# Optimization experiments

Measured on AMD Instinct MI355X. Metric: run time of the kernel, lower is better.

The kernel has to match this reference:

```python
import jax, jax.numpy as jnp
import numpy as np

I, H, O = 256, 512, 256  # input_size, hidden_size, output_size
B, S = 4096, 50


def _lstm_cell(x_t, h, c, Wih, Whh, bih, bhh):
    # torch gate order: i, f, g, o
    gates = x_t @ Wih.T + h @ Whh.T + bih + bhh  # [B, 4H]
    i, f, g, o = jnp.split(gates, 4, axis=-1)
    i = jax.nn.sigmoid(i)
    f = jax.nn.sigmoid(f)
    g = jnp.tanh(g)
    o = jax.nn.sigmoid(o)
    c_new = f * c + i * g
    h_new = o * jnp.tanh(c_new)
    return h_new, c_new


def setup_inputs() -> dict:
    key = jax.random.key(0)
    ks = jax.random.split(key, 12)
    s_i = 1.0 / np.sqrt(H)  # torch LSTM/Linear init scale
    u = lambda k, shape: jax.random.uniform(k, shape, jnp.float32, -s_i, s_i)
    return {
        "x": jax.random.normal(ks[0], (B, S, I), jnp.float32),
        "enc_Wih": u(ks[1], (4 * H, I)),
        "enc_Whh": u(ks[2], (4 * H, H)),
        "enc_bih": u(ks[3], (4 * H,)),
        "enc_bhh": u(ks[4], (4 * H,)),
        "dec_Wih": u(ks[5], (4 * H, I)),
        "dec_Whh": u(ks[6], (4 * H, H)),
        "dec_bih": u(ks[7], (4 * H,)),
        "dec_bhh": u(ks[8], (4 * H,)),
        "fc_W": u(ks[9], (O, H)),
        "fc_b": u(ks[10], (O,)),
        "target_seq_length": 20,
    }


def reference(x, enc_Wih, enc_Whh, enc_bih, enc_bhh,
              dec_Wih, dec_Whh, dec_bih, dec_bhh,
              fc_W, fc_b, target_seq_length):
    batch = x.shape[0]
    h0 = jnp.zeros((batch, H), x.dtype)
    c0 = jnp.zeros((batch, H), x.dtype)

    # ---- encoder: scan over time ----
    def enc_step(carry, x_t):
        h, c = carry
        h, c = _lstm_cell(x_t, h, c, enc_Wih, enc_Whh, enc_bih, enc_bhh)
        return (h, c), None

    (h, c), _ = jax.lax.scan(enc_step, (h0, c0), jnp.swapaxes(x, 0, 1))

    dec_in0 = jnp.zeros((batch, I), x.dtype)

    def dec_step(carry, _):
        h, c, inp = carry
        h, c = _lstm_cell(inp, h, c, dec_Wih, dec_Whh, dec_bih, dec_bhh)
        out = h @ fc_W.T + fc_b  # [B, O]
        return (h, c, out), out

    _, outs = jax.lax.scan(dec_step, (h, c, dec_in0), None,
                           length=target_seq_length)
    return jnp.swapaxes(outs, 0, 1)  # [B, T, O]
```

## Files before the change

### kernel.cpp

```cpp
#include <hip/hip_runtime.h>

#define I_SZ 256
#define H_SZ 512
#define O_SZ 256
#define B_SZ 4096
#define S_SZ 50
#define T_SZ 20
#define G4H  2048
#define BH   ((size_t)B_SZ * H_SZ)
#define NB   512
#define NSTEP (S_SZ + T_SZ)

#define PAD 72
#define PAD_H 36

typedef _Float16 half8 __attribute__((ext_vector_type(8)));
typedef float f32x4 __attribute__((ext_vector_type(4)));

__device__ __forceinline__ float sigm(float x) {
    return 1.0f / (1.0f + __expf(-x));
}
__device__ __forceinline__ float tanh_fast(float x) {
    float e = __expf(2.0f * x);
    return 1.0f - 2.0f / (e + 1.0f);
}

#define GLDS(gp, lp, aux) __builtin_amdgcn_global_load_lds(                 \
    (const __attribute__((address_space(1))) void*)(gp),                    \
    (__attribute__((address_space(3))) void*)(lp), 16, 0, (aux))

#define MEMFENCE asm volatile("" ::: "memory")

__global__ void k_zeroN(unsigned* p, int n) {
    int i = blockIdx.x * blockDim.x + threadIdx.x;
    if (i < n) p[i] = 0u;
}

__global__ void k_cvt(const float* __restrict__ src, _Float16* __restrict__ dst, int n) {
    int i = blockIdx.x * blockDim.x + threadIdx.x;
    if (i < n) dst[i] = (_Float16)src[i];
}

__global__ void k_bias_combine(const float* __restrict__ a, const float* __restrict__ b,
                               float* __restrict__ dst, int n) {
    int i = blockIdx.x * blockDim.x + threadIdx.x;
    if (i < n) dst[i] = a[i] + b[i];
}

__global__ __launch_bounds__(256) void k_cvt_x(const float* __restrict__ x,
                                               _Float16* __restrict__ xT) {
    size_t idx = ((size_t)blockIdx.x * 256 + threadIdx.x) * 8;
    int i = (int)(idx & 255);
    int s = (int)((idx >> 8) % S_SZ);
    size_t b = idx / (256 * S_SZ);
    float4 v0 = *(const float4*)(x + idx);
    float4 v1 = *(const float4*)(x + idx + 4);
    half8 hv;
    hv[0] = (_Float16)v0.x; hv[1] = (_Float16)v0.y;
    hv[2] = (_Float16)v0.z; hv[3] = (_Float16)v0.w;
    hv[4] = (_Float16)v1.x; hv[5] = (_Float16)v1.y;
    hv[6] = (_Float16)v1.z; hv[7] = (_Float16)v1.w;
    *(half8*)(xT + (((size_t)s * B_SZ + b) * I_SZ + i)) = hv;
}

__global__ void k_wenc(const float* __restrict__ eWih, const float* __restrict__ eWhh,
                       _Float16* __restrict__ Wenc) {
    int idx = blockIdx.x * blockDim.x + threadIdx.x;
    int r = idx / 768, col = idx % 768;
    float v = (col < 256) ? eWih[(size_t)r * 256 + col] : eWhh[(size_t)r * 512 + col - 256];
    Wenc[idx] = (_Float16)v;
}

__global__ __launch_bounds__(256) void k_wd(
    const float* __restrict__ dWhh, const float* __restrict__ dWih,
    const float* __restrict__ fcW, _Float16* __restrict__ Wd)
{
    __shared__ float sA[8][256];
    const int tid = threadIdx.x;
    const int r0 = blockIdx.x * 8;
    {
        int linear = tid * 8;
        int row = linear >> 8, col = linear & 255;
        const float4* p = (const float4*)(dWih + (size_t)(r0 + row) * 256 + col);
        float4 v0 = p[0], v1 = p[1];
        *(float4*)&sA[row][col]     = v0;
        *(float4*)&sA[row][col + 4] = v1;
    }
    __syncthreads();
    float acc[8][2] = {};
    const int k = tid;
    for (int i = 0; i < 256; ++i) {
        float w0 = fcW[(size_t)i * 512 + k];
        float w1 = fcW[(size_t)i * 512 + k + 256];
        #pragma unroll
        for (int rr = 0; rr < 8; ++rr) {
            float a = sA[rr][i];
            acc[rr][0] += a * w0;
            acc[rr][1] += a * w1;
        }
    }
    #pragma unroll
    for (int rr = 0; rr < 8; ++rr) {
        size_t base = (size_t)(r0 + rr) * 512;
        Wd[base + k]       = (_Float16)(dWhh[base + k]       + acc[rr][0]);
        Wd[base + k + 256] = (_Float16)(dWhh[base + k + 256] + acc[rr][1]);
    }
}

__global__ __launch_bounds__(256) void k_bd(
    const float* __restrict__ dWih, const float* __restrict__ fcb,
    const float* __restrict__ db, float* __restrict__ bd)
{
    __shared__ float sf[256];
    const int tid = threadIdx.x;
    sf[tid] = fcb[tid];
    __syncthreads();
    int r = blockIdx.x * 256 + tid;
    float acc = db[r];
    const float* row = dWih + (size_t)r * 256;
    for (int o = 0; o < 256; o += 4) {
        float4 v = *(const float4*)(row + o);
        acc += v.x * sf[o] + v.y * sf[o + 1] + v.z * sf[o + 2] + v.w * sf[o + 3];
    }
    bd[r] = acc;
}

__global__ __launch_bounds__(256, 2) void k_lstm_all(
    const _Float16* __restrict__ xT,
    const _Float16* __restrict__ Wenc,
    const _Float16* __restrict__ dWhh_h,
    const _Float16* __restrict__ Wd,
    const float* __restrict__ eb, const float* __restrict__ db,
    const float* __restrict__ bd,
    _Float16* __restrict__ h0buf, _Float16* __restrict__ h1buf,
    _Float16* __restrict__ hseq,
    unsigned* __restrict__ bar)
{
    __shared__ _Float16 lds[2][2][128 * 64];

    const int tid = threadIdx.x;
    const int xcd = blockIdx.x & 7, slot = blockIdx.x >> 3;
    const int mb = xcd * 4 + (slot >> 4);
    const int jb = slot & 15;
    const int m0 = mb * 128, j0 = jb * 32;
    unsigned* grp = bar + mb * 16;

    const int wv = tid >> 6, lane = tid & 63, lrow = lane & 15, lk8 = (lane >> 4) * 8;
    const int wm = wv >> 1, wn = wv & 1;

    const int colb  = (lane & 7) * 16;
    const int scolh = (colb ^ (((lane >> 3) & 7) << 4)) >> 1;
    int rowq[4], growq[4];
    #pragma unroll
    for (int q = 0; q < 4; ++q) {
        int r = q * 32 + wv * 8 + (lane >> 3);
        rowq[q] = r;
        growq[q] = ((r >> 4) & 3) * H_SZ + j0 + (r >> 6) * 16 + (r & 15);
    }

    float ebj[4], dbj[4], bdj[4];
    #pragma unroll
    for (int nf = 0; nf < 4; ++nf) {
        int col = nf * H_SZ + j0 + wn * 16 + lrow;
        ebj[nf] = eb[col]; dbj[nf] = db[col]; bdj[nf] = bd[col];
    }

    float creg[4][4];

    for (int step = 0; step < NSTEP; ++step) {
        const _Float16* xsrc; const _Float16* hin; const _Float16* W;
        _Float16* hout; int wstride, nx, niter;
        if (step < S_SZ) {
            xsrc = xT + (size_t)step * B_SZ * I_SZ;
            W = Wenc; wstride = 768; nx = 4;
            niter = (step == 0) ? 4 : 12;
            hin  = (step == 0) ? nullptr : ((step & 1) ? h0buf : h1buf);
            hout = (step == S_SZ - 1) ? hseq : ((step & 1) ? h1buf : h0buf);
        } else {
            int t = step - S_SZ;
            xsrc = nullptr; nx = 0; niter = 8; wstride = 512;
            W = (t == 0) ? dWhh_h : Wd;
            hin  = hseq + (size_t)t * BH;
            hout = hseq + (size_t)(t + 1) * BH;
        }

        auto wait_group = [&]() {
            MEMFENCE;
            if (tid == 0) {
                unsigned target = (unsigned)step * 16u;
                while (__hip_atomic_load(grp, __ATOMIC_RELAXED, __HIP_MEMORY_SCOPE_AGENT) < target)
                    __builtin_amdgcn_s_sleep(1);
            }
            __builtin_amdgcn_s_barrier();
            MEMFENCE;
        };

        auto stage = [&](int buf, int it) {
            const int koffW = it * 64;
            #pragma unroll
            for (int q = 0; q < 4; ++q) {
                const _Float16* gb = W + (size_t)growq[q] * wstride + koffW + scolh;
                GLDS(gb, &lds[buf][1][(q * 256 + wv * 64) * 8], 0);
            }
            if (it < nx) {
                #pragma unroll
                for (int q = 0; q < 4; ++q) {
                    const _Float16* ga = xsrc + (size_t)(m0 + rowq[q]) * I_SZ + it * 64 + scolh;
                    GLDS(ga, &lds[buf][0][(q * 256 + wv * 64) * 8], 0);
                }
            } else {
                #pragma unroll
                for (int q = 0; q < 4; ++q) {
                    const _Float16* ga = hin + (size_t)(m0 + rowq[q]) * H_SZ + (it - nx) * 64 + scolh;
                    GLDS(ga, &lds[buf][0][(q * 256 + wv * 64) * 8], 17);
                }
            }
        };

        f32x4 acc[4][4];
        #pragma unroll
        for (int mf = 0; mf < 4; ++mf)
            #pragma unroll
            for (int nf = 0; nf < 4; ++nf) {
                f32x4 z = {0.f, 0.f, 0.f, 0.f};
                acc[mf][nf] = z;
            }

        auto compute = [&](int buf) {
            #pragma unroll
            for (int kc = 0; kc < 2; ++kc) {
                const int cb = (kc * 32 + lk8) * 2;
                const int sc = (cb ^ ((lrow & 7) << 4)) >> 1;
                half8 a[4], b[4];
                #pragma unroll
                for (int mf = 0; mf < 4; ++mf)
                    a[mf] = *(const half8*)&lds[buf][0][(wm * 64 + mf * 16 + lrow) * 64 + sc];
                #pragma unroll
                for (int nf = 0; nf < 4; ++nf)
                    b[nf] = *(const half8*)&lds[buf][1][(wn * 64 + nf * 16 + lrow) * 64 + sc];
                #pragma unroll
                for (int mf = 0; mf < 4; ++mf)
                    #pragma unroll
                    for (int nf = 0; nf < 4; ++nf)
                        acc[mf][nf] = __builtin_amdgcn_mfma_f32_16x16x32_f16(a[mf], b[nf], acc[mf][nf], 0, 0, 0);
            }
        };

        if (step > 0 && nx == 0) wait_group();
        stage(0, 0);
        int buf = 0;
        for (int it = 0; it < niter; ++it) {
            if (it + 1 < niter) {
                if (step > 0 && nx > 0 && it + 1 == nx) wait_group();
                stage(buf ^ 1, it + 1);
                asm volatile("s_waitcnt vmcnt(8)" ::: "memory");
            } else {
                asm volatile("s_waitcnt vmcnt(0)" ::: "memory");
            }
            __builtin_amdgcn_s_barrier();
            MEMFENCE;
            compute(buf);
            MEMFENCE;
            __builtin_amdgcn_s_barrier();
            MEMFENCE;
            buf ^= 1;
        }

        float bj[4];
        #pragma unroll
        for (int nf = 0; nf < 4; ++nf)
            bj[nf] = (step < S_SZ) ? ebj[nf] : ((step == S_SZ) ? dbj[nf] : bdj[nf]);

        _Float16* hsm = &lds[0][0][0];
        const int lc = wn * 16 + lrow;
        #pragma unroll
        for (int mf = 0; mf < 4; ++mf)
            #pragma unroll
            for (int r = 0; r < 4; ++r) {
                int lr = wm * 64 + mf * 16 + (lane >> 4) * 4 + r;
                float gi = acc[mf][0][r] + bj[0];
                float gf = acc[mf][1][r] + bj[1];
                float gg = acc[mf][2][r] + bj[2];
                float go = acc[mf][3][r] + bj[3];
                float cold = (step == 0) ? 0.0f : creg[mf][r];
                float cn = sigm(gf) * cold + sigm(gi) * tanh_fast(gg);
                creg[mf][r] = cn;
                hsm[lr * PAD_H + lc] = (_Float16)(sigm(go) * tanh_fast(cn));
            }
        __syncthreads();
        {
            int rr = tid >> 3, k = tid & 7;
            #pragma unroll
            for (int q = 0; q < 4; ++q) {
                int r = rr + q * 32;
                unsigned long long v = *(const unsigned long long*)&hsm[r * PAD_H + k * 4];
                unsigned long long* dst =
                    (unsigned long long*)(hout + (size_t)(m0 + r) * H_SZ + j0) + k;
                __hip_atomic_store(dst, v, __ATOMIC_RELAXED, __HIP_MEMORY_SCOPE_AGENT);
            }
        }

        if (step != NSTEP - 1) {
            __syncthreads();
            if (tid == 0)
                __hip_atomic_fetch_add(grp, 1u, __ATOMIC_RELAXED, __HIP_MEMORY_SCOPE_AGENT);
        }
    }
}

__global__ __launch_bounds__(256) void k_fc(
    const _Float16* __restrict__ hseq1,
    const _Float16* __restrict__ W,
    const float* __restrict__ bias,
    float* __restrict__ out)
{
    __shared__ _Float16 Asm[128][PAD];
    __shared__ _Float16 Bsm[128][PAD];

    const int tid = threadIdx.x;
    const int m0 = blockIdx.x * 128;
    const int t  = blockIdx.y;
    const int n0 = blockIdx.z * 128;
    const int wv = tid >> 6, lane = tid & 63, lrow = lane & 15, lk = (lane >> 4) * 8;
    const int wm = wv >> 1, wn = wv & 1;

    f32x4 acc[4][4] = {};

    const int srow = tid >> 3, skc = (tid & 7) * 8;
    const _Float16* A = hseq1 + (size_t)t * BH;

    for (int k0 = 0; k0 < H_SZ; k0 += 64) {
        __syncthreads();
        #pragma unroll
        for (int q = 0; q < 4; ++q) {
            int r = srow + q * 32;
            *(half8*)&Asm[r][skc] = *(const half8*)(A + (size_t)(m0 + r) * H_SZ + k0 + skc);
        }
        #pragma unroll
        for (int q = 0; q < 4; ++q) {
            int rr = srow + q * 32;
            *(half8*)&Bsm[rr][skc] = *(const half8*)(W + (size_t)(n0 + rr) * H_SZ + k0 + skc);
        }
        __syncthreads();
        #pragma unroll
        for (int kc = 0; kc < 64; kc += 32) {
            half8 a[4], b[4];
            #pragma unroll
            for (int mf = 0; mf < 4; ++mf) a[mf] = *(const half8*)&Asm[wm * 64 + mf * 16 + lrow][kc + lk];
            #pragma unroll
            for (int nf = 0; nf < 4; ++nf) b[nf] = *(const half8*)&Bsm[wn * 64 + nf * 16 + lrow][kc + lk];
            #pragma unroll
            for (int mf = 0; mf < 4; ++mf)
                #pragma unroll
                for (int nf = 0; nf < 4; ++nf)
                    acc[mf][nf] = __builtin_amdgcn_mfma_f32_16x16x32_f16(a[mf], b[nf], acc[mf][nf], 0, 0, 0);
        }
    }

    #pragma unroll
    for (int mf = 0; mf < 4; ++mf)
        #pragma unroll
        for (int nf = 0; nf < 4; ++nf) {
            int o = n0 + wn * 64 + nf * 16 + lrow;
            float bv = bias[o];
            #pragma unroll
            for (int r = 0; r < 4; ++r) {
                int m = m0 + wm * 64 + mf * 16 + (lane >> 4) * 4 + r;
                out[(size_t)m * (T_SZ * O_SZ) + (size_t)t * O_SZ + o] = acc[mf][nf][r] + bv;
            }
        }
}

extern "C" void kernel_launch(void* const* d_in, const int* in_sizes, int n_in,
                              void* d_out, int out_size, void* d_ws, size_t ws_size,
                              hipStream_t stream) {
    (void)in_sizes; (void)n_in; (void)out_size; (void)ws_size;

    const float* x    = (const float*)d_in[0];
    const float* eWih = (const float*)d_in[1];
    const float* eWhh = (const float*)d_in[2];
    const float* ebih = (const float*)d_in[3];
    const float* ebhh = (const float*)d_in[4];
    const float* dWih = (const float*)d_in[5];
    const float* dWhh = (const float*)d_in[6];
    const float* dbih = (const float*)d_in[7];
    const float* dbhh = (const float*)d_in[8];
    const float* fcW  = (const float*)d_in[9];
    const float* fcb  = (const float*)d_in[10];
    float* out = (float*)d_out;
    char* ws = (char*)d_ws;

    size_t off = 0;
    auto alloc = [&](size_t bytes) -> void* {
        void* p = ws + off;
        off += (bytes + 255) & ~(size_t)255;
        return p;
    };
    _Float16* xT     = (_Float16*)alloc((size_t)S_SZ * B_SZ * I_SZ * 2);
    _Float16* Wenc   = (_Float16*)alloc((size_t)G4H * (I_SZ + H_SZ) * 2);
    _Float16* dWhh_h = (_Float16*)alloc((size_t)G4H * H_SZ * 2);
    _Float16* Wd     = (_Float16*)alloc((size_t)G4H * H_SZ * 2);
    _Float16* fcW_h  = (_Float16*)alloc((size_t)O_SZ * H_SZ * 2);
    float*    eb     = (float*)alloc(G4H * 4);
    float*    db     = (float*)alloc(G4H * 4);
    float*    bd     = (float*)alloc(G4H * 4);
    _Float16* h0     = (_Float16*)alloc(BH * 2);
    _Float16* h1     = (_Float16*)alloc(BH * 2);
    _Float16* hseq   = (_Float16*)alloc((size_t)(T_SZ + 1) * BH * 2);
    unsigned* bar    = (unsigned*)alloc(32 * 16 * 4);

    const int nWhh = G4H * H_SZ;
    const int nFc  = O_SZ * H_SZ;
    const size_t nX = (size_t)B_SZ * S_SZ * I_SZ;

    k_zeroN<<<2, 256, 0, stream>>>(bar, 32 * 16);
    k_cvt_x<<<(int)(nX / 8 / 256), 256, 0, stream>>>(x, xT);
    k_wenc<<<(G4H * 768) / 256, 256, 0, stream>>>(eWih, eWhh, Wenc);
    k_cvt<<<(nWhh + 255) / 256, 256, 0, stream>>>(dWhh, dWhh_h, nWhh);
    k_cvt<<<(nFc + 255) / 256, 256, 0, stream>>>(fcW, fcW_h, nFc);
    k_bias_combine<<<8, 256, 0, stream>>>(ebih, ebhh, eb, G4H);
    k_bias_combine<<<8, 256, 0, stream>>>(dbih, dbhh, db, G4H);
    k_wd<<<256, 256, 0, stream>>>(dWhh, dWih, fcW, Wd);
    k_bd<<<8, 256, 0, stream>>>(dWih, fcb, db, bd);

    k_lstm_all<<<NB, 256, 0, stream>>>(xT, Wenc, dWhh_h, Wd, eb, db, bd,
                                       h0, h1, hseq, bar);

    k_fc<<<dim3(B_SZ / 128, T_SZ, O_SZ / 128), 256, 0, stream>>>(
        hseq + BH, fcW_h, fcb, out);
}
```

Baseline: 1.331 ms.

## Split LSTM loop into specialized phases with per-step hidden buffers and cached pointers

Splits the single generic time-step loop into three specialized loops (first encoder step, remaining encoder steps, decoder steps), each fully unrolled with compile-time iteration counts. Per-lane global pointers are precomputed once instead of recomputing row and stride math every stage. The encoder hidden state now goes to a distinct buffer per step instead of ping-ponging between two, so hidden loads drop the cache-policy bits (aux 17) and use default caching. This avoids write-after-read hazards on reused buffers, at the cost of much more workspace memory and larger code.

```diff
diff --git a/kernel.cpp b/kernel.cpp
--- a/kernel.cpp
+++ b/kernel.cpp
@@ -9,7 +9,6 @@
 #define G4H  2048
 #define BH   ((size_t)B_SZ * H_SZ)
 #define NB   512
-#define NSTEP (S_SZ + T_SZ)
 
 #define PAD 72
 #define PAD_H 36
@@ -25,9 +24,9 @@
     return 1.0f - 2.0f / (e + 1.0f);
 }
 
-#define GLDS(gp, lp, aux) __builtin_amdgcn_global_load_lds(                 \
+#define GLDS(gp, lp) __builtin_amdgcn_global_load_lds(                      \
     (const __attribute__((address_space(1))) void*)(gp),                    \
-    (__attribute__((address_space(3))) void*)(lp), 16, 0, (aux))
+    (__attribute__((address_space(3))) void*)(lp), 16, 0, 0)
 
 #define MEMFENCE asm volatile("" ::: "memory")
 
@@ -132,7 +131,7 @@
     const _Float16* __restrict__ Wd,
     const float* __restrict__ eb, const float* __restrict__ db,
     const float* __restrict__ bd,
-    _Float16* __restrict__ h0buf, _Float16* __restrict__ h1buf,
+    _Float16* __restrict__ henc,
     _Float16* __restrict__ hseq,
     unsigned* __restrict__ bar)
 {
@@ -150,12 +149,20 @@
 
     const int colb  = (lane & 7) * 16;
     const int scolh = (colb ^ (((lane >> 3) & 7) << 4)) >> 1;
-    int rowq[4], growq[4];
+    const _Float16* wEncQ[4]; const _Float16* wD0Q[4]; const _Float16* wDQ[4];
+    const _Float16* xQ[4];
+    unsigned aOffQ[4];
+    int ldsQ[4];
     #pragma unroll
     for (int q = 0; q < 4; ++q) {
         int r = q * 32 + wv * 8 + (lane >> 3);
-        rowq[q] = r;
-        growq[q] = ((r >> 4) & 3) * H_SZ + j0 + (r >> 6) * 16 + (r & 15);
+        int grow = ((r >> 4) & 3) * H_SZ + j0 + (r >> 6) * 16 + (r & 15);
+        wEncQ[q] = Wenc   + (size_t)grow * 768 + scolh;
+        wD0Q[q]  = dWhh_h + (size_t)grow * 512 + scolh;
+        wDQ[q]   = Wd     + (size_t)grow * 512 + scolh;
+        xQ[q]    = xT + (size_t)(m0 + r) * I_SZ + scolh;
+        aOffQ[q] = (unsigned)((m0 + r) * H_SZ) + scolh;
+        ldsQ[q]  = (q * 256 + wv * 64) * 8;
     }
 
     float ebj[4], dbj[4], bdj[4];
@@ -167,110 +174,41 @@
 
     float creg[4][4];
 
-    for (int step = 0; step < NSTEP; ++step) {
-        const _Float16* xsrc; const _Float16* hin; const _Float16* W;
-        _Float16* hout; int wstride, nx, niter;
-        if (step < S_SZ) {
-            xsrc = xT + (size_t)step * B_SZ * I_SZ;
-            W = Wenc; wstride = 768; nx = 4;
-            niter = (step == 0) ? 4 : 12;
-            hin  = (step == 0) ? nullptr : ((step & 1) ? h0buf : h1buf);
-            hout = (step == S_SZ - 1) ? hseq : ((step & 1) ? h1buf : h0buf);
-        } else {
-            int t = step - S_SZ;
-            xsrc = nullptr; nx = 0; niter = 8; wstride = 512;
-            W = (t == 0) ? dWhh_h : Wd;
-            hin  = hseq + (size_t)t * BH;
-            hout = hseq + (size_t)(t + 1) * BH;
-        }
-
-        auto wait_group = [&]() {
-            MEMFENCE;
-            if (tid == 0) {
-                unsigned target = (unsigned)step * 16u;
-                while (__hip_atomic_load(grp, __ATOMIC_RELAXED, __HIP_MEMORY_SCOPE_AGENT) < target)
-                    __builtin_amdgcn_s_sleep(1);
-            }
-            __builtin_amdgcn_s_barrier();
-            MEMFENCE;
-        };
-
-        auto stage = [&](int buf, int it) {
-            const int koffW = it * 64;
-            #pragma unroll
-            for (int q = 0; q < 4; ++q) {
-                const _Float16* gb = W + (size_t)growq[q] * wstride + koffW + scolh;
-                GLDS(gb, &lds[buf][1][(q * 256 + wv * 64) * 8], 0);
-            }
-            if (it < nx) {
-                #pragma unroll
-                for (int q = 0; q < 4; ++q) {
-                    const _Float16* ga = xsrc + (size_t)(m0 + rowq[q]) * I_SZ + it * 64 + scolh;
-                    GLDS(ga, &lds[buf][0][(q * 256 + wv * 64) * 8], 0);
-                }
-            } else {
-                #pragma unroll
-                for (int q = 0; q < 4; ++q) {
-                    const _Float16* ga = hin + (size_t)(m0 + rowq[q]) * H_SZ + (it - nx) * 64 + scolh;
-                    GLDS(ga, &lds[buf][0][(q * 256 + wv * 64) * 8], 17);
-                }
-            }
-        };
-
-        f32x4 acc[4][4];
-        #pragma unroll
-        for (int mf = 0; mf < 4; ++mf)
-            #pragma unroll
-            for (int nf = 0; nf < 4; ++nf) {
-                f32x4 z = {0.f, 0.f, 0.f, 0.f};
-                acc[mf][nf] = z;
-            }
-
-        auto compute = [&](int buf) {
-            #pragma unroll
-            for (int kc = 0; kc < 2; ++kc) {
-                const int cb = (kc * 32 + lk8) * 2;
-                const int sc = (cb ^ ((lrow & 7) << 4)) >> 1;
-                half8 a[4], b[4];
-                #pragma unroll
-                for (int mf = 0; mf < 4; ++mf)
-                    a[mf] = *(const half8*)&lds[buf][0][(wm * 64 + mf * 16 + lrow) * 64 + sc];
+    auto wait_group = [&](unsigned target) {
+        MEMFENCE;
+        if (tid == 0) {
+            while (__hip_atomic_load(grp, __ATOMIC_RELAXED, __HIP_MEMORY_SCOPE_AGENT) < target)
+                __builtin_amdgcn_s_sleep(1);
+        }
+        __builtin_amdgcn_s_barrier();
+        MEMFENCE;
+    };
+    auto arrive = [&]() {
+        __syncthreads();
+        if (tid == 0)
+            __hip_atomic_fetch_add(grp, 1u, __ATOMIC_RELAXED, __HIP_MEMORY_SCOPE_AGENT);
+    };
+
+    auto compute = [&](int buf, f32x4 (&acc)[4][4]) {
+        #pragma unroll
+        for (int kc = 0; kc < 2; ++kc) {
+            const int sc = (((kc * 32 + lk8) * 2) ^ ((lrow & 7) << 4)) >> 1;
+            half8 a[4], b[4];
+            #pragma unroll
+            for (int mf = 0; mf < 4; ++mf)
+                a[mf] = *(const half8*)&lds[buf][0][(wm * 64 + mf * 16 + lrow) * 64 + sc];
+            #pragma unroll
+            for (int nf = 0; nf < 4; ++nf)
+                b[nf] = *(const half8*)&lds[buf][1][(wn * 64 + nf * 16 + lrow) * 64 + sc];
+            #pragma unroll
+            for (int mf = 0; mf < 4; ++mf)
                 #pragma unroll
                 for (int nf = 0; nf < 4; ++nf)
-                    b[nf] = *(const half8*)&lds[buf][1][(wn * 64 + nf * 16 + lrow) * 64 + sc];
-                #pragma unroll
-                for (int mf = 0; mf < 4; ++mf)
-                    #pragma unroll
-                    for (int nf = 0; nf < 4; ++nf)
-                        acc[mf][nf] = __builtin_amdgcn_mfma_f32_16x16x32_f16(a[mf], b[nf], acc[mf][nf], 0, 0, 0);
-            }
-        };
-
-        if (step > 0 && nx == 0) wait_group();
-        stage(0, 0);
-        int buf = 0;
-        for (int it = 0; it < niter; ++it) {
-            if (it + 1 < niter) {
-                if (step > 0 && nx > 0 && it + 1 == nx) wait_group();
-                stage(buf ^ 1, it + 1);
-                asm volatile("s_waitcnt vmcnt(8)" ::: "memory");
-            } else {
-                asm volatile("s_waitcnt vmcnt(0)" ::: "memory");
-            }
-            __builtin_amdgcn_s_barrier();
-            MEMFENCE;
-            compute(buf);
-            MEMFENCE;
-            __builtin_amdgcn_s_barrier();
-            MEMFENCE;
-            buf ^= 1;
-        }
-
-        float bj[4];
-        #pragma unroll
-        for (int nf = 0; nf < 4; ++nf)
-            bj[nf] = (step < S_SZ) ? ebj[nf] : ((step == S_SZ) ? dbj[nf] : bdj[nf]);
-
+                    acc[mf][nf] = __builtin_amdgcn_mfma_f32_16x16x32_f16(a[mf], b[nf], acc[mf][nf], 0, 0, 0);
+        }
+    };
+
+    auto epilogue = [&](f32x4 (&acc)[4][4], const float (&bj)[4], _Float16* hout, bool first) {
         _Float16* hsm = &lds[0][0][0];
         const int lc = wn * 16 + lrow;
         #pragma unroll
@@ -282,29 +220,108 @@
                 float gf = acc[mf][1][r] + bj[1];
                 float gg = acc[mf][2][r] + bj[2];
                 float go = acc[mf][3][r] + bj[3];
-                float cold = (step == 0) ? 0.0f : creg[mf][r];
+                float cold = first ? 0.0f : creg[mf][r];
                 float cn = sigm(gf) * cold + sigm(gi) * tanh_fast(gg);
                 creg[mf][r] = cn;
                 hsm[lr * PAD_H + lc] = (_Float16)(sigm(go) * tanh_fast(cn));
             }
         __syncthreads();
-        {
-            int rr = tid >> 3, k = tid & 7;
-            #pragma unroll
-            for (int q = 0; q < 4; ++q) {
-                int r = rr + q * 32;
-                unsigned long long v = *(const unsigned long long*)&hsm[r * PAD_H + k * 4];
-                unsigned long long* dst =
-                    (unsigned long long*)(hout + (size_t)(m0 + r) * H_SZ + j0) + k;
-                __hip_atomic_store(dst, v, __ATOMIC_RELAXED, __HIP_MEMORY_SCOPE_AGENT);
+        int rr = tid >> 3, k = tid & 7;
+        #pragma unroll
+        for (int q = 0; q < 4; ++q) {
+            int r = rr + q * 32;
+            unsigned long long v = *(const unsigned long long*)&hsm[r * PAD_H + k * 4];
+            unsigned long long* dst =
+                (unsigned long long*)(hout + (size_t)(m0 + r) * H_SZ + j0) + k;
+            __hip_atomic_store(dst, v, __ATOMIC_RELAXED, __HIP_MEMORY_SCOPE_AGENT);
+        }
+    };
+
+    {
+        f32x4 acc[4][4] = {};
+        #pragma unroll
+        for (int q = 0; q < 4; ++q) { GLDS(xQ[q], &lds[0][0][ldsQ[q]]); GLDS(wEncQ[q], &lds[0][1][ldsQ[q]]); }
+        #pragma unroll
+        for (int it = 0; it < 4; ++it) {
+            if (it < 3) {
+                #pragma unroll
+                for (int q = 0; q < 4; ++q) {
+                    GLDS(xQ[q] + (it + 1) * 64, &lds[(it + 1) & 1][0][ldsQ[q]]);
+                    GLDS(wEncQ[q] + (it + 1) * 64, &lds[(it + 1) & 1][1][ldsQ[q]]);
+                }
+                asm volatile("s_waitcnt vmcnt(8)" ::: "memory");
+            } else {
+                asm volatile("s_waitcnt vmcnt(0)" ::: "memory");
             }
-        }
-
-        if (step != NSTEP - 1) {
-            __syncthreads();
-            if (tid == 0)
-                __hip_atomic_fetch_add(grp, 1u, __ATOMIC_RELAXED, __HIP_MEMORY_SCOPE_AGENT);
-        }
+            __builtin_amdgcn_s_barrier(); MEMFENCE;
+            compute(it & 1, acc);
+            MEMFENCE; __builtin_amdgcn_s_barrier(); MEMFENCE;
+        }
+        epilogue(acc, ebj, henc, true);
+        arrive();
+    }
+
+    for (int s = 1; s < S_SZ; ++s) {
+        const size_t xoff = (size_t)s * B_SZ * I_SZ;
+        const _Float16* hin = henc + (size_t)(s - 1) * BH;
+        _Float16* hout = (s == S_SZ - 1) ? hseq : henc + (size_t)s * BH;
+        f32x4 acc[4][4] = {};
+        #pragma unroll
+        for (int q = 0; q < 4; ++q) { GLDS(xQ[q] + xoff, &lds[0][0][ldsQ[q]]); GLDS(wEncQ[q], &lds[0][1][ldsQ[q]]); }
+        #pragma unroll
+        for (int it = 0; it < 12; ++it) {
+            if (it < 11) {
+                if (it == 3) wait_group((unsigned)s * 16u);
+                #pragma unroll
+                for (int q = 0; q < 4; ++q) {
+                    if (it + 1 < 4) GLDS(xQ[q] + xoff + (it + 1) * 64, &lds[(it + 1) & 1][0][ldsQ[q]]);
+                    else            GLDS(hin + aOffQ[q] + (it - 3) * 64, &lds[(it + 1) & 1][0][ldsQ[q]]);
+                    GLDS(wEncQ[q] + (it + 1) * 64, &lds[(it + 1) & 1][1][ldsQ[q]]);
+                }
+                asm volatile("s_waitcnt vmcnt(8)" ::: "memory");
+            } else {
+                asm volatile("s_waitcnt vmcnt(0)" ::: "memory");
+            }
+            __builtin_amdgcn_s_barrier(); MEMFENCE;
+            compute(it & 1, acc);
+            MEMFENCE; __builtin_amdgcn_s_barrier(); MEMFENCE;
+        }
+        epilogue(acc, ebj, hout, false);
+        arrive();
+    }
+
+    for (int t = 0; t < T_SZ; ++t) {
+        const _Float16* hin = hseq + (size_t)t * BH;
+        _Float16* hout = hseq + (size_t)(t + 1) * BH;
+        const _Float16* wq[4];
+        float bj[4];
+        #pragma unroll
+        for (int q = 0; q < 4; ++q) wq[q] = t ? wDQ[q] : wD0Q[q];
+        #pragma unroll
+        for (int nf = 0; nf < 4; ++nf) bj[nf] = t ? bdj[nf] : dbj[nf];
+
+        wait_group((unsigned)(S_SZ + t) * 16u);
+        f32x4 acc[4][4] = {};
+        #pragma unroll
+        for (int q = 0; q < 4; ++q) { GLDS(hin + aOffQ[q], &lds[0][0][ldsQ[q]]); GLDS(wq[q], &lds[0][1][ldsQ[q]]); }
+        #pragma unroll
+        for (int it = 0; it < 8; ++it) {
+            if (it < 7) {
+                #pragma unroll
+                for (int q = 0; q < 4; ++q) {
+                    GLDS(hin + aOffQ[q] + (it + 1) * 64, &lds[(it + 1) & 1][0][ldsQ[q]]);
+                    GLDS(wq[q] + (it + 1) * 64, &lds[(it + 1) & 1][1][ldsQ[q]]);
+                }
+                asm volatile("s_waitcnt vmcnt(8)" ::: "memory");
+            } else {
+                asm volatile("s_waitcnt vmcnt(0)" ::: "memory");
+            }
+            __builtin_amdgcn_s_barrier(); MEMFENCE;
+            compute(it & 1, acc);
+            MEMFENCE; __builtin_amdgcn_s_barrier(); MEMFENCE;
+        }
+        epilogue(acc, bj, hout, false);
+        if (t != T_SZ - 1) arrive();
     }
 }
 
@@ -404,8 +421,7 @@
     float*    eb     = (float*)alloc(G4H * 4);
     float*    db     = (float*)alloc(G4H * 4);
     float*    bd     = (float*)alloc(G4H * 4);
-    _Float16* h0     = (_Float16*)alloc(BH * 2);
-    _Float16* h1     = (_Float16*)alloc(BH * 2);
+    _Float16* henc   = (_Float16*)alloc((size_t)(S_SZ - 1) * BH * 2);
     _Float16* hseq   = (_Float16*)alloc((size_t)(T_SZ + 1) * BH * 2);
     unsigned* bar    = (unsigned*)alloc(32 * 16 * 4);
 
@@ -424,7 +440,7 @@
     k_bd<<<8, 256, 0, stream>>>(dWih, fcb, db, bd);
 
     k_lstm_all<<<NB, 256, 0, stream>>>(xT, Wenc, dWhh_h, Wd, eb, db, bd,
-                                       h0, h1, hseq, bar);
+                                       henc, hseq, bar);
 
     k_fc<<<dim3(B_SZ / 128, T_SZ, O_SZ / 128), 256, 0, stream>>>(
         hseq + BH, fcW_h, fcb, out);
```

Measured after the change: 1.271 ms. 1.05x faster.
